# Kernel optimization log

Hardware: AMD Instinct MI355X
Metric: run time of the kernel (lower is better)

Reference implementation:

```python
import jax, jax.numpy as jnp
import numpy as np

EPS = 1e-5

def layernorm(x, g, b):
    mu = x.mean(-1, keepdims=True)
    var = ((x - mu) ** 2).mean(-1, keepdims=True)
    return (x - mu) / jnp.sqrt(var + EPS) * g + b

def segment_softmax(logits, seg, num_seg):
    # logits: [E, H, Q]; softmax over edges sharing the same target segment
    m = jax.ops.segment_max(logits, seg, num_segments=num_seg)
    ex = jnp.exp(logits - m[seg])
    s = jax.ops.segment_sum(ex, seg, num_segments=num_seg)
    return ex / s[seg]

def mha(x, Kw, Qw, Vw, tgt, src, n_tgt):
    # x: [N_src, C]; Kw/Vw: [H, C, D]; Qw: [H, Q, D]
    xK = jnp.einsum('nc,hcd->hnd', x, Kw)
    alpha = jnp.einsum('hqd,hnd->hqn', Qw, xK)            # [H, Q, N_src]
    a_e = alpha.transpose(2, 0, 1)[src]                   # [E, H, Q] per-edge logits
    w = segment_softmax(a_e, tgt, n_tgt)                  # sparse softmax over sources per target
    xV = jnp.einsum('nc,hcd->hnd', x, Vw)                 # [H, N_src, D]
    msg = w[..., None] * xV.transpose(1, 0, 2)[src][:, :, None, :]  # [E, H, Q, D]
    return jax.ops.segment_sum(msg, tgt, num_segments=n_tgt)        # [n_tgt, H, Q, D]

def block(x, tgt, src, n_tgt, Kw, Qw, Vw, g0, b0, W1, W2, g1, b1):
    Qn = Qw.shape[1]
    h = mha(x, Kw, Qw, Vw, tgt, src, n_tgt) + Qw          # [n_tgt, H, Q, D]
    h = h.transpose(0, 2, 1, 3).reshape(n_tgt, Qn, -1)    # [n_tgt, Q, hidden]
    h = layernorm(h, g0, b0)
    m = jax.nn.relu(jax.nn.relu(h @ W1) @ W2)             # MLP(Linear,ReLU,Linear) + outer ReLU
    h = layernorm(h + m, g1, b1)
    return h.sum(axis=1)                                  # [n_tgt, hidden]

def setup_inputs() -> dict:
    key = jax.random.key(0)
    ks = jax.random.split(key, 12)
    N, M, E, C, H, Q, D = 50000, 20000, 1000000, 128, 4, 1, 32
    HID = H * D
    s = 0.1
    inp = {
        'x_0': jax.random.normal(ks[0], (N, C), jnp.float32),
        'node_idx': jax.random.randint(ks[1], (E,), 0, N),
        'hedge_idx': jax.random.randint(ks[2], (E,), 0, M),
        'n_nodes': N,
        'n_hedges': M,
        'v2e_K': jax.random.normal(ks[3], (H, C, D), jnp.float32) * s,
        'v2e_Q': jax.random.normal(ks[4], (H, Q, D), jnp.float32) * s,
        'v2e_V': jax.random.normal(ks[5], (H, C, D), jnp.float32) * s,
        'v2e_ln0_g': jnp.ones((HID,), jnp.float32),
        'v2e_ln0_b': jnp.zeros((HID,), jnp.float32),
        'v2e_W1': jax.random.normal(ks[6], (HID, HID), jnp.float32) * s,
        'v2e_W2': jax.random.normal(ks[7], (HID, HID), jnp.float32) * s,
        'v2e_ln1_g': jnp.ones((HID,), jnp.float32),
        'v2e_ln1_b': jnp.zeros((HID,), jnp.float32),
        'e2v_K': jax.random.normal(ks[8], (H, HID, D), jnp.float32) * s,
        'e2v_Q': jax.random.normal(ks[9], (H, Q, D), jnp.float32) * s,
        'e2v_V': jax.random.normal(ks[10], (H, HID, D), jnp.float32) * s,
        'e2v_ln0_g': jnp.ones((HID,), jnp.float32),
        'e2v_ln0_b': jnp.zeros((HID,), jnp.float32),
        'e2v_W1': jax.random.normal(ks[11], (HID, HID), jnp.float32) * s,
        'e2v_W2': jax.random.normal(jax.random.fold_in(key, 99), (HID, HID), jnp.float32) * s,
        'e2v_ln1_g': jnp.ones((HID,), jnp.float32),
        'e2v_ln1_b': jnp.zeros((HID,), jnp.float32),
    }
    return inp

def reference(x_0, node_idx, hedge_idx, n_nodes, n_hedges,
              v2e_K, v2e_Q, v2e_V, v2e_ln0_g, v2e_ln0_b, v2e_W1, v2e_W2, v2e_ln1_g, v2e_ln1_b,
              e2v_K, e2v_Q, e2v_V, e2v_ln0_g, e2v_ln0_b, e2v_W1, e2v_W2, e2v_ln1_g, e2v_ln1_b):
    # vertex -> hyperedge: neighborhood = incidence^T, targets = hyperedges, sources = nodes
    x_1 = jax.nn.relu(block(x_0, hedge_idx, node_idx, n_hedges,
                            v2e_K, v2e_Q, v2e_V, v2e_ln0_g, v2e_ln0_b,
                            v2e_W1, v2e_W2, v2e_ln1_g, v2e_ln1_b))
    # hyperedge -> vertex: neighborhood = incidence, targets = nodes, sources = hyperedges
    x_0_out = jax.nn.relu(block(x_1, node_idx, hedge_idx, n_nodes,
                                e2v_K, e2v_Q, e2v_V, e2v_ln0_g, e2v_ln0_b,
                                e2v_W1, e2v_W2, e2v_ln1_g, e2v_ln1_b))
    return x_0_out, x_1
```

## Files before the change

kernel.cpp:

```cpp
#include <hip/hip_runtime.h>
#include <math.h>

typedef __attribute__((ext_vector_type(8))) short bf16x8;
typedef __attribute__((ext_vector_type(4))) float f32x4;

#define CSR_P 256

__device__ __forceinline__ unsigned short f2bf(float f){
  union { float f; unsigned int u; } c; c.f = f;
  unsigned int u = c.u;
  u += 0x7fff + ((u >> 16) & 1);
  return (unsigned short)(u >> 16);
}
__device__ __forceinline__ float bf2f(unsigned short h){
  union { unsigned int u; float f; } c; c.u = ((unsigned int)h) << 16;
  return c.f;
}

__device__ __forceinline__ float wsum64(float v){
  #pragma unroll
  for (int off = 32; off > 0; off >>= 1) v += __shfl_xor(v, off, 64);
  return v;
}

__global__ __launch_bounds__(256) void prephist_kernel(
    const int* __restrict__ tgt0, int NB0, const int* __restrict__ tgt1, int NB1, int E,
    int* __restrict__ counts0, int* __restrict__ counts1,
    const float* __restrict__ K0, const float* __restrict__ Q0, const float* __restrict__ V0,
    const float* __restrict__ W10, const float* __restrict__ W20,
    const float* __restrict__ K1, const float* __restrict__ Q1, const float* __restrict__ V1,
    const float* __restrict__ W11, const float* __restrict__ W21,
    unsigned short* __restrict__ btV0, unsigned short* __restrict__ btkq0,
    unsigned short* __restrict__ btW10, unsigned short* __restrict__ btW20,
    unsigned short* __restrict__ btV1, unsigned short* __restrict__ btkq1,
    unsigned short* __restrict__ btW11, unsigned short* __restrict__ btW21,
    int* __restrict__ cursors){
  if (blockIdx.x >= CSR_P){
    int pb = blockIdx.x - CSR_P;
    if (pb == 0 && blockIdx.y == 0 && threadIdx.x == 0){ cursors[0] = 0; cursors[1] = 0; }
    const float *K, *Q, *V, *W1, *W2;
    unsigned short *btV, *btkq, *btW1, *btW2;
    if (blockIdx.y == 0){ K=K0; Q=Q0; V=V0; W1=W10; W2=W20; btV=btV0; btkq=btkq0; btW1=btW10; btW2=btW20; }
    else                { K=K1; Q=Q1; V=V1; W1=W11; W2=W21; btV=btV1; btkq=btkq1; btW1=btW11; btW2=btW21; }
    int i = pb * 256 + threadIdx.x;
    if (i < 512){
      int h = i >> 7, c = i & 127;
      const float* Kp = K + (size_t)h * 4096 + (size_t)c * 32;
      const float* Qp = Q + h * 32;
      float s = 0.f;
      #pragma unroll
      for (int d = 0; d < 32; ++d) s += Kp[d] * Qp[d];
      unsigned short hi = f2bf(s);
      btkq[h * 128 + c]       = hi;
      btkq[(4 + h) * 128 + c] = f2bf(s - bf2f(hi));
      return;
    }
    int j = i - 512;
    if (j < 16384){
      int n = j >> 7, k = j & 127;
      int h = n >> 5, d = n & 31;
      btV[j] = f2bf(V[(size_t)h * 4096 + (size_t)k * 32 + d]);
      return;
    }
    j -= 16384;
    if (j < 16384){
      int n = j >> 7, k = j & 127;
      btW1[j] = f2bf(W1[(size_t)k * 128 + n]);
      return;
    }
    j -= 16384;
    if (j < 16384){
      int n = j >> 7, k = j & 127;
      btW2[j] = f2bf(W2[(size_t)k * 128 + n]);
    }
    return;
  }
  const int* tgt; int NB; int* counts;
  if (blockIdx.y == 0){ tgt = tgt0; NB = NB0; counts = counts0; }
  else                { tgt = tgt1; NB = NB1; counts = counts1; }
  __shared__ int hist[256];
  for (int i = threadIdx.x; i < NB; i += 256) hist[i] = 0;
  __syncthreads();
  int chunk = (E + CSR_P - 1) / CSR_P;
  int b0 = blockIdx.x * chunk, b1 = min(b0 + chunk, E);
  for (int e = b0 + threadIdx.x; e < b1; e += 256)
    atomicAdd(&hist[tgt[e] >> 8], 1);
  __syncthreads();
  for (int i = threadIdx.x; i < NB; i += 256)
    counts[i * CSR_P + blockIdx.x] = hist[i];
}

__global__ __launch_bounds__(256) void bscan_kernel(const int* __restrict__ counts0, int NB0,
                                                    const int* __restrict__ counts1,
                                                    int* __restrict__ blkoff0, int* __restrict__ blkoff1,
                                                    int* __restrict__ btot0, int* __restrict__ btot1,
                                                    int* __restrict__ base0, int* __restrict__ base1,
                                                    int* __restrict__ cursors){
  int i = blockIdx.x;
  const int* counts; int* blkoff; int* btot; int* bbase; int* cur; int b;
  if (i < NB0){ counts = counts0; blkoff = blkoff0; btot = btot0; bbase = base0; cur = &cursors[0]; b = i; }
  else        { counts = counts1; blkoff = blkoff1; btot = btot1; bbase = base1; cur = &cursors[1]; b = i - NB0; }
  __shared__ int wtmp[5];
  int tid = threadIdx.x, lane = tid & 63, wv = tid >> 6;
  int c = counts[b * CSR_P + tid];
  int s = c;
  #pragma unroll
  for (int off = 1; off < 64; off <<= 1){
    int t = __shfl_up(s, off, 64);
    if (lane >= off) s += t;
  }
  if (lane == 63) wtmp[wv] = s;
  __syncthreads();
  if (tid == 0){
    int a0 = wtmp[0], a1 = wtmp[1], a2 = wtmp[2], a3 = wtmp[3];
    wtmp[0] = 0; wtmp[1] = a0; wtmp[2] = a0 + a1; wtmp[3] = a0 + a1 + a2;
    int total = a0 + a1 + a2 + a3;
    wtmp[4] = total;
    btot[b] = total;
    int padded = ((total + 3) & ~3) + 1024;
    bbase[b] = atomicAdd(cur, padded);
  }
  __syncthreads();
  blkoff[b * CSR_P + tid] = s - c + wtmp[wv];
}

__global__ __launch_bounds__(256) void scatter2_kernel(
    const int* __restrict__ tgt0, const int* __restrict__ src0, int NB0,
    const int* __restrict__ base0, const int* __restrict__ blkoff0, int* __restrict__ pairs0,
    const int* __restrict__ tgt1, const int* __restrict__ src1, int NB1,
    const int* __restrict__ base1, const int* __restrict__ blkoff1, int* __restrict__ pairs1,
    int E){
  const int *tgt, *src, *bbase, *boff; int NB; int* pairs;
  if (blockIdx.y == 0){ tgt=tgt0; src=src0; bbase=base0; boff=blkoff0; NB=NB0; pairs=pairs0; }
  else                { tgt=tgt1; src=src1; bbase=base1; boff=blkoff1; NB=NB1; pairs=pairs1; }
  __shared__ int cur[256];
  for (int i = threadIdx.x; i < NB; i += 256)
    cur[i] = bbase[i] + boff[i * CSR_P + blockIdx.x];
  __syncthreads();
  int chunk = (E + CSR_P - 1) / CSR_P;
  int b0 = blockIdx.x * chunk, b1 = min(b0 + chunk, E);
  for (int e = b0 + threadIdx.x; e < b1; e += 256){
    int t = tgt[e];
    int pos = atomicAdd(&cur[t >> 8], 1);
    pairs[pos] = ((t & 255) << 24) | src[e];
  }
}

__global__ __launch_bounds__(1024) void build2_kernel(
    const int* __restrict__ base0, const int* __restrict__ btot0, int NB0,
    const int* __restrict__ pairs0, int n0, int d0,
    int* __restrict__ rp0, int* __restrict__ kc0, int* __restrict__ col0,
    const int* __restrict__ base1, const int* __restrict__ btot1, int NB1,
    const int* __restrict__ pairs1, int n1, int d1,
    int* __restrict__ rp1, int* __restrict__ kc1, int* __restrict__ col1){
  int b = blockIdx.x;
  const int *bbase, *bt; const int* pairs; int n_tgt, dummy;
  int *rowptr, *kcnt, *col;
  if (blockIdx.y == 0){
    if (b >= NB0) return;
    bbase=base0; bt=btot0; pairs=pairs0; n_tgt=n0; dummy=d0; rowptr=rp0; kcnt=kc0; col=col0;
  } else {
    if (b >= NB1) return;
    bbase=base1; bt=btot1; pairs=pairs1; n_tgt=n1; dummy=d1; rowptr=rp1; kcnt=kc1; col=col1;
  }
  __shared__ int hist2[2048];
  __shared__ int cur2[2048];
  __shared__ int hist[256];
  __shared__ int excl[256];
  int tid = threadIdx.x;
  int start = bbase[b];
  int end   = start + bt[b];
  for (int i = tid; i < 2048; i += 1024) hist2[i] = 0;
  __syncthreads();
  for (int e = start + tid; e < end; e += 1024){
    int p = pairs[e];
    atomicAdd(&hist2[(((p >> 24) & 255) << 3) | ((p & 0xFFFFFF) >> 13)], 1);
  }
  __syncthreads();
  if (tid < 256){
    int run = 0;
    #pragma unroll
    for (int t = 0; t < 8; ++t){ cur2[tid * 8 + t] = run; run += hist2[tid * 8 + t]; }
    hist[tid] = run;
  }
  __syncthreads();
  if (tid < 64){
    int lane = tid;
    int p0 = (hist[4 * lane]     + 3) & ~3;
    int p1 = (hist[4 * lane + 1] + 3) & ~3;
    int p2 = (hist[4 * lane + 2] + 3) & ~3;
    int p3 = (hist[4 * lane + 3] + 3) & ~3;
    int tsum = p0 + p1 + p2 + p3;
    int s = tsum;
    #pragma unroll
    for (int off = 1; off < 64; off <<= 1){
      int t = __shfl_up(s, off, 64);
      if (lane >= off) s += t;
    }
    int e0 = s - tsum;
    excl[4 * lane]     = e0;
    excl[4 * lane + 1] = e0 + p0;
    excl[4 * lane + 2] = e0 + p0 + p1;
    excl[4 * lane + 3] = e0 + p0 + p1 + p2;
  }
  __syncthreads();
  int t0 = b << 8;
  int valid = min(256, n_tgt - t0);
  if (tid < 256){
    int e0 = excl[tid];
    #pragma unroll
    for (int t = 0; t < 8; ++t) cur2[tid * 8 + t] += e0;
  }
  for (int i = tid; i < valid; i += 1024){
    rowptr[t0 + i] = start + excl[i];
    kcnt[t0 + i]   = (hist[i] + 3) & ~3;
  }
  __syncthreads();
  for (int e = start + tid; e < end; e += 1024){
    int p = pairs[e];
    int s = p & 0xFFFFFF;
    int pos = atomicAdd(&cur2[(((p >> 24) & 255) << 3) | (s >> 13)], 1);
    col[start + pos] = s;
  }
  __syncthreads();
  for (int i = tid; i < valid; i += 1024){
    int hc = hist[i], pc = (hc + 3) & ~3;
    int base = start + excl[i];
    for (int j = hc; j < pc; ++j) col[base + j] = dummy;
  }
}

__global__ __launch_bounds__(256) void gemm_xvl(const float* __restrict__ x,
                                                const unsigned short* __restrict__ btV,
                                                const unsigned short* __restrict__ btkq,
                                                unsigned short* __restrict__ xv,
                                                float* __restrict__ expl, int R){
  __shared__ unsigned short As[64 * 136];
  __shared__ unsigned short Bs[144 * 136];
  int tid = threadIdx.x;
  int row0 = blockIdx.x * 64;

  #pragma unroll
  for (int i = 0; i < 16; ++i){
    int f = tid + i * 256;
    int n = f >> 5, c4 = f & 31;
    *(ushort4*)&Bs[n * 136 + c4 * 4] = *(const ushort4*)(btV + n * 128 + c4 * 4);
  }
  {
    int n = tid >> 5, c4 = tid & 31;
    *(ushort4*)&Bs[(128 + n) * 136 + c4 * 4] = *(const ushort4*)(btkq + n * 128 + c4 * 4);
  }
  #pragma unroll
  for (int i = 0; i < 8; ++i){
    int f = tid + i * 256;
    int r = f >> 5, c4 = f & 31;
    float4 v = make_float4(0.f, 0.f, 0.f, 0.f);
    if (row0 + r < R) v = *(const float4*)(x + (size_t)(row0 + r) * 128 + c4 * 4);
    ushort4 h;
    h.x = f2bf(v.x); h.y = f2bf(v.y); h.z = f2bf(v.z); h.w = f2bf(v.w);
    *(ushort4*)&As[r * 136 + c4 * 4] = h;
  }
  __syncthreads();

  int lane = tid & 63, wv = tid >> 6;
  int m = lane & 15, quad = lane >> 4;
  f32x4 acc[9];
  #pragma unroll
  for (int j = 0; j < 9; ++j) acc[j] = (f32x4){0.f, 0.f, 0.f, 0.f};

  #pragma unroll
  for (int q = 0; q < 4; ++q){
    bf16x8 a = *(const bf16x8*)&As[(wv * 16 + m) * 136 + q * 32 + quad * 8];
    #pragma unroll
    for (int j = 0; j < 9; ++j){
      bf16x8 b = *(const bf16x8*)&Bs[(j * 16 + m) * 136 + q * 32 + quad * 8];
      acc[j] = __builtin_amdgcn_mfma_f32_16x16x32_bf16(a, b, acc[j], 0, 0, 0);
    }
  }

  #pragma unroll
  for (int j = 0; j < 8; ++j){
    int colc = j * 16 + m;
    #pragma unroll
    for (int r = 0; r < 4; ++r){
      int gr = row0 + wv * 16 + quad * 4 + r;
      if (gr <= R) xv[(size_t)gr * 128 + colc] = f2bf(acc[j][r]);
    }
  }
  #pragma unroll
  for (int r = 0; r < 4; ++r){
    int gr = row0 + wv * 16 + quad * 4 + r;
    float lg = acc[8][r] + __shfl_xor(acc[8][r], 4, 64);
    if (m < 4 && gr <= R)
      expl[(size_t)gr * 4 + m] = (gr == R) ? 0.f : __expf(lg);
  }
}

__global__ __launch_bounds__(256) void agg_kernel(const int* __restrict__ rowptr,
                                                  const int* __restrict__ kcnt,
                                                  const int* __restrict__ col,
                                                  const float* __restrict__ expl,
                                                  const unsigned short* __restrict__ xV,
                                                  const float* __restrict__ qvec,
                                                  const float* __restrict__ g0,
                                                  const float* __restrict__ b0,
                                                  unsigned short* __restrict__ hb_out,
                                                  int n_tgt){
  int wv_id = __builtin_amdgcn_readfirstlane(threadIdx.x >> 6);
  int wid = (blockIdx.x << 2) + wv_id;
  if (wid >= n_tgt) return;
  int lane = threadIdx.x & 63;
  int half = lane >> 5;
  int c    = lane & 31;
  unsigned hh = (unsigned)(c >> 3);
  int beg = rowptr[wid];
  int k   = kcnt[wid];

  const uint2* xv64 = (const uint2*)xV;
  float acc0 = 0.f, acc1 = 0.f, acc2 = 0.f, acc3 = 0.f, sumw = 0.f;
  #pragma unroll 2
  for (int e = 0; e < k; e += 4){
    int4 cc = *(const int4*)(col + beg + e);
    #pragma unroll
    for (int p = 0; p < 2; ++p){
      int sA = p ? cc.z : cc.x;
      int sB = p ? cc.w : cc.y;
      int se = half ? sB : sA;
      float a  = expl[((unsigned)se << 2) + hh];
      uint2 v  = xv64[((unsigned)se << 5) + (unsigned)c];
      union { unsigned u; float f; } t0, t1, t2, t3;
      t0.u = v.x << 16;          t1.u = v.x & 0xffff0000u;
      t2.u = v.y << 16;          t3.u = v.y & 0xffff0000u;
      sumw += a;
      acc0 += a * t0.f;  acc1 += a * t1.f;
      acc2 += a * t2.f;  acc3 += a * t3.f;
    }
  }
  sumw += __shfl_xor(sumw, 32, 64);
  acc0 += __shfl_xor(acc0, 32, 64);
  acc1 += __shfl_xor(acc1, 32, 64);
  acc2 += __shfl_xor(acc2, 32, 64);
  acc3 += __shfl_xor(acc3, 32, 64);

  float inv = (sumw > 0.f) ? 1.f / sumw : 0.f;
  acc0 *= inv; acc1 *= inv; acc2 *= inv; acc3 *= inv;

  float4 q4 = *(const float4*)(qvec + 4 * c);
  acc0 += q4.x; acc1 += q4.y; acc2 += q4.z; acc3 += q4.w;

  float mean = wsum64(acc0 + acc1 + acc2 + acc3) * (1.f / 256.f);
  float d0 = acc0 - mean, d1 = acc1 - mean, d2 = acc2 - mean, d3 = acc3 - mean;
  float var = wsum64(d0 * d0 + d1 * d1 + d2 * d2 + d3 * d3) * (1.f / 256.f);
  float rstd = rsqrtf(var + 1e-5f);
  float4 g4 = *(const float4*)(g0 + 4 * c);
  float4 b4 = *(const float4*)(b0 + 4 * c);
  float o0 = d0 * rstd * g4.x + b4.x;
  float o1 = d1 * rstd * g4.y + b4.y;
  float o2 = d2 * rstd * g4.z + b4.z;
  float o3 = d3 * rstd * g4.w + b4.w;
  if (half == 0){
    uint2 pk;
    pk.x = ((unsigned)f2bf(o1) << 16) | (unsigned)f2bf(o0);
    pk.y = ((unsigned)f2bf(o3) << 16) | (unsigned)f2bf(o2);
    *(uint2*)(hb_out + 128 * (size_t)wid + 4 * c) = pk;
  }
}

__global__ __launch_bounds__(256) void mfma_mlp_ln(const unsigned short* __restrict__ A,
                                                   const unsigned short* __restrict__ Bt1,
                                                   const unsigned short* __restrict__ Bt2,
                                                   const float* __restrict__ g,
                                                   const float* __restrict__ b,
                                                   float* __restrict__ outp, int R){
  __shared__ unsigned short As[64 * 136];
  __shared__ unsigned short Bs[128 * 136];
  int tid = threadIdx.x;
  int row0 = blockIdx.x * 64;

  #pragma unroll
  for (int i = 0; i < 16; ++i){
    int f = tid + i * 256;
    int n = f >> 5, c4 = f & 31;
    *(ushort4*)&Bs[n * 136 + c4 * 4] = *(const ushort4*)(Bt1 + n * 128 + c4 * 4);
  }
  #pragma unroll
  for (int i = 0; i < 8; ++i){
    int f = tid + i * 256;
    int r = f >> 5, c4 = f & 31;
    ushort4 v = make_ushort4(0, 0, 0, 0);
    if (row0 + r < R) v = *(const ushort4*)(A + (size_t)(row0 + r) * 128 + c4 * 4);
    *(ushort4*)&As[r * 136 + c4 * 4] = v;
  }
  __syncthreads();

  int lane = tid & 63, wv = tid >> 6;
  int m = lane & 15, quad = lane >> 4;
  f32x4 acc[8];
  #pragma unroll
  for (int j = 0; j < 8; ++j) acc[j] = (f32x4){0.f, 0.f, 0.f, 0.f};

  #pragma unroll
  for (int q = 0; q < 4; ++q){
    bf16x8 a = *(const bf16x8*)&As[(wv * 16 + m) * 136 + q * 32 + quad * 8];
    #pragma unroll
    for (int j = 0; j < 8; ++j){
      bf16x8 b8 = *(const bf16x8*)&Bs[(j * 16 + m) * 136 + q * 32 + quad * 8];
      acc[j] = __builtin_amdgcn_mfma_f32_16x16x32_bf16(a, b8, acc[j], 0, 0, 0);
    }
  }

  float res[4][8];
  #pragma unroll
  for (int r = 0; r < 4; ++r)
    #pragma unroll
    for (int j = 0; j < 8; ++j)
      res[r][j] = bf2f(As[(wv * 16 + quad * 4 + r) * 136 + j * 16 + m]);
  __syncthreads();

  #pragma unroll
  for (int j = 0; j < 8; ++j){
    #pragma unroll
    for (int r = 0; r < 4; ++r)
      As[(wv * 16 + quad * 4 + r) * 136 + j * 16 + m] = f2bf(fmaxf(acc[j][r], 0.f));
  }
  #pragma unroll
  for (int i = 0; i < 16; ++i){
    int f = tid + i * 256;
    int n = f >> 5, c4 = f & 31;
    *(ushort4*)&Bs[n * 136 + c4 * 4] = *(const ushort4*)(Bt2 + n * 128 + c4 * 4);
  }
  __syncthreads();

  #pragma unroll
  for (int j = 0; j < 8; ++j) acc[j] = (f32x4){0.f, 0.f, 0.f, 0.f};
  #pragma unroll
  for (int q = 0; q < 4; ++q){
    bf16x8 a = *(const bf16x8*)&As[(wv * 16 + m) * 136 + q * 32 + quad * 8];
    #pragma unroll
    for (int j = 0; j < 8; ++j){
      bf16x8 b8 = *(const bf16x8*)&Bs[(j * 16 + m) * 136 + q * 32 + quad * 8];
      acc[j] = __builtin_amdgcn_mfma_f32_16x16x32_bf16(a, b8, acc[j], 0, 0, 0);
    }
  }

  float gv[8], bv[8];
  #pragma unroll
  for (int j = 0; j < 8; ++j){ gv[j] = g[j * 16 + m]; bv[j] = b[j * 16 + m]; }

  #pragma unroll
  for (int r = 0; r < 4; ++r){
    int gr = row0 + wv * 16 + quad * 4 + r;
    if (gr >= R) continue;
    float v[8];
    float s = 0.f;
    #pragma unroll
    for (int j = 0; j < 8; ++j){
      float mm = fmaxf(acc[j][r], 0.f);
      v[j] = res[r][j] + mm;
      s += v[j];
    }
    s += __shfl_xor(s, 1, 64); s += __shfl_xor(s, 2, 64);
    s += __shfl_xor(s, 4, 64); s += __shfl_xor(s, 8, 64);
    float mean = s * (1.f / 128.f);
    float s2 = 0.f;
    #pragma unroll
    for (int j = 0; j < 8; ++j){ v[j] -= mean; s2 += v[j] * v[j]; }
    s2 += __shfl_xor(s2, 1, 64); s2 += __shfl_xor(s2, 2, 64);
    s2 += __shfl_xor(s2, 4, 64); s2 += __shfl_xor(s2, 8, 64);
    float rstd = rsqrtf(s2 * (1.f / 128.f) + 1e-5f);
    #pragma unroll
    for (int j = 0; j < 8; ++j)
      outp[(size_t)gr * 128 + j * 16 + m] = fmaxf(v[j] * rstd * gv[j] + bv[j], 0.f);
  }
}

struct Ws {
  float *expl;
  unsigned short *btV0, *btkq0, *btW10, *btW20, *btV1, *btkq1, *btW11, *btW21, *xv, *hb;
};

static void run_stage(const float* x_f32, int R_src,
                      const int* rowptr, const int* kcnt, const int* col, int n_tgt,
                      const unsigned short* btV, const unsigned short* btkq,
                      const unsigned short* btW1, const unsigned short* btW2,
                      const float* Qw, const float* g0, const float* b0,
                      const float* g1, const float* b1,
                      float* out, const Ws& ws, hipStream_t stream)
{
  gemm_xvl<<<(R_src + 1 + 63) / 64, 256, 0, stream>>>(x_f32, btV, btkq, ws.xv, ws.expl, R_src);
  agg_kernel<<<(n_tgt + 3) / 4, 256, 0, stream>>>(rowptr, kcnt, col, ws.expl, ws.xv,
                                                  Qw, g0, b0, ws.hb, n_tgt);
  mfma_mlp_ln<<<(n_tgt + 63) / 64, 256, 0, stream>>>(ws.hb, btW1, btW2, g1, b1, out, n_tgt);
}

extern "C" void kernel_launch(void* const* d_in, const int* in_sizes, int n_in,
                              void* d_out, int out_size, void* d_ws, size_t ws_size,
                              hipStream_t stream)
{
  const float* x0        = (const float*)d_in[0];
  const int*   node_idx  = (const int*)d_in[1];
  const int*   hedge_idx = (const int*)d_in[2];
  const float* v2e_K = (const float*)d_in[5];
  const float* v2e_Q = (const float*)d_in[6];
  const float* v2e_V = (const float*)d_in[7];
  const float* v2e_g0 = (const float*)d_in[8];
  const float* v2e_b0 = (const float*)d_in[9];
  const float* v2e_W1 = (const float*)d_in[10];
  const float* v2e_W2 = (const float*)d_in[11];
  const float* v2e_g1 = (const float*)d_in[12];
  const float* v2e_b1 = (const float*)d_in[13];
  const float* e2v_K = (const float*)d_in[14];
  const float* e2v_Q = (const float*)d_in[15];
  const float* e2v_V = (const float*)d_in[16];
  const float* e2v_g0 = (const float*)d_in[17];
  const float* e2v_b0 = (const float*)d_in[18];
  const float* e2v_W1 = (const float*)d_in[19];
  const float* e2v_W2 = (const float*)d_in[20];
  const float* e2v_g1 = (const float*)d_in[21];
  const float* e2v_b1 = (const float*)d_in[22];

  int N = in_sizes[0] / 128;
  int E = in_sizes[1];
  int M = out_size / 128 - N;

  float* out_x0 = (float*)d_out;
  float* out_x1 = (float*)d_out + (size_t)N * 128;

  size_t off = 0;
  char* base = (char*)d_ws;
  auto alloc = [&](size_t bytes) -> void* {
    void* p = base + off;
    off += (bytes + 255) & ~(size_t)255;
    return p;
  };
  int NB0 = (M + 255) >> 8;
  int NB1 = (N + 255) >> 8;
  int NBmax = NB1 > NB0 ? NB1 : NB0;
  size_t capP = (size_t)E + 1024 * (size_t)NBmax + 64;

  Ws ws;
  ws.btV0  = (unsigned short*)alloc(16384 * 2);
  ws.btkq0 = (unsigned short*)alloc(1024 * 2);
  ws.btW10 = (unsigned short*)alloc(16384 * 2);
  ws.btW20 = (unsigned short*)alloc(16384 * 2);
  ws.btV1  = (unsigned short*)alloc(16384 * 2);
  ws.btkq1 = (unsigned short*)alloc(1024 * 2);
  ws.btW11 = (unsigned short*)alloc(16384 * 2);
  ws.btW21 = (unsigned short*)alloc(16384 * 2);
  ws.expl  = (float*)alloc(((size_t)N + 1) * 4 * 4);
  size_t uoff = off;
  ws.xv    = (unsigned short*)alloc(((size_t)N + 1) * 128 * 2);
  ws.hb    = (unsigned short*)alloc((size_t)N * 128 * 2);
  int* pairs0  = (int*)(base + uoff);
  int* pairs1  = pairs0 + capP;
  int* counts0 = pairs1 + capP;
  int* counts1 = counts0 + 256 * CSR_P;
  int* blkoff0 = counts1 + 256 * CSR_P;
  int* blkoff1 = blkoff0 + 256 * CSR_P;
  int* btot0   = blkoff1 + 256 * CSR_P;
  int* btot1   = btot0 + 256;
  int* base0   = btot1 + 256;
  int* base1   = base0 + 256;
  int* cursors = base1 + 256;
  int* rowptr0 = (int*)alloc((size_t)M * 4);
  int* kcnt0   = (int*)alloc((size_t)M * 4);
  int* col0    = (int*)alloc(capP * 4);
  int* rowptr1 = (int*)alloc((size_t)N * 4);
  int* kcnt1   = (int*)alloc((size_t)N * 4);
  int* col1    = (int*)alloc(capP * 4);
  (void)ws_size; (void)n_in;

  prephist_kernel<<<dim3(CSR_P + 194, 2), 256, 0, stream>>>(
      hedge_idx, NB0, node_idx, NB1, E, counts0, counts1,
      v2e_K, v2e_Q, v2e_V, v2e_W1, v2e_W2,
      e2v_K, e2v_Q, e2v_V, e2v_W1, e2v_W2,
      ws.btV0, ws.btkq0, ws.btW10, ws.btW20,
      ws.btV1, ws.btkq1, ws.btW11, ws.btW21, cursors);

  bscan_kernel<<<NB0 + NB1, 256, 0, stream>>>(counts0, NB0, counts1,
                                              blkoff0, blkoff1, btot0, btot1,
                                              base0, base1, cursors);
  scatter2_kernel<<<dim3(CSR_P, 2), 256, 0, stream>>>(
      hedge_idx, node_idx, NB0, base0, blkoff0, pairs0,
      node_idx, hedge_idx, NB1, base1, blkoff1, pairs1, E);
  build2_kernel<<<dim3(NBmax, 2), 1024, 0, stream>>>(
      base0, btot0, NB0, pairs0, M, N, rowptr0, kcnt0, col0,
      base1, btot1, NB1, pairs1, N, M, rowptr1, kcnt1, col1);

  run_stage(x0, N, rowptr0, kcnt0, col0, M,
            ws.btV0, ws.btkq0, ws.btW10, ws.btW20,
            v2e_Q, v2e_g0, v2e_b0, v2e_g1, v2e_b1,
            out_x1, ws, stream);

  run_stage(out_x1, M, rowptr1, kcnt1, col1, N,
            ws.btV1, ws.btkq1, ws.btW11, ws.btW21,
            e2v_Q, e2v_g0, e2v_b0, e2v_g1, e2v_b1,
            out_x0, ws, stream);
}
```

Baseline: 286.2 us.

## Fuse scatter with first GEMM, split aggregation by channel halves, move LN0 into MLP

Merges the CSR scatter kernel and the first-stage xV/logit GEMM into one launch, so GEMM blocks can run alongside the scatter blocks. The aggregation kernel now runs in two launches, each covering 64 of the 128 channels with 32-bit gathers. This is meant to shrink the per-pass working set and cache footprint, at the cost of re-reading col and expl twice. The Q-bias add and first layernorm move out of aggregation into the MLP kernel's A-tile load, computed with one-pass mean and variance. Scratch buffers no longer alias the xv region because the GEMM now runs concurrently with the scatter.

```diff
diff --git a/kernel.cpp b/kernel.cpp
--- a/kernel.cpp
+++ b/kernel.cpp
@@ -15,12 +15,6 @@
 __device__ __forceinline__ float bf2f(unsigned short h){
   union { unsigned int u; float f; } c; c.u = ((unsigned int)h) << 16;
   return c.f;
-}
-
-__device__ __forceinline__ float wsum64(float v){
-  #pragma unroll
-  for (int off = 32; off > 0; off >>= 1) v += __shfl_xor(v, off, 64);
-  return v;
 }
 
 __global__ __launch_bounds__(256) void prephist_kernel(
@@ -124,26 +118,112 @@
   blkoff[b * CSR_P + tid] = s - c + wtmp[wv];
 }
 
-__global__ __launch_bounds__(256) void scatter2_kernel(
+__device__ __forceinline__ void gemm_xvl_body(unsigned short* As, unsigned short* Bs,
+                                              const float* __restrict__ x,
+                                              const unsigned short* __restrict__ btV,
+                                              const unsigned short* __restrict__ btkq,
+                                              unsigned short* __restrict__ xv,
+                                              float* __restrict__ expl, int R, int bx){
+  int tid = threadIdx.x;
+  int row0 = bx * 64;
+
+  #pragma unroll
+  for (int i = 0; i < 16; ++i){
+    int f = tid + i * 256;
+    int n = f >> 5, c4 = f & 31;
+    *(ushort4*)&Bs[n * 136 + c4 * 4] = *(const ushort4*)(btV + n * 128 + c4 * 4);
+  }
+  {
+    int n = tid >> 5, c4 = tid & 31;
+    *(ushort4*)&Bs[(128 + n) * 136 + c4 * 4] = *(const ushort4*)(btkq + n * 128 + c4 * 4);
+  }
+  #pragma unroll
+  for (int i = 0; i < 8; ++i){
+    int f = tid + i * 256;
+    int r = f >> 5, c4 = f & 31;
+    float4 v = make_float4(0.f, 0.f, 0.f, 0.f);
+    if (row0 + r < R) v = *(const float4*)(x + (size_t)(row0 + r) * 128 + c4 * 4);
+    ushort4 h;
+    h.x = f2bf(v.x); h.y = f2bf(v.y); h.z = f2bf(v.z); h.w = f2bf(v.w);
+    *(ushort4*)&As[r * 136 + c4 * 4] = h;
+  }
+  __syncthreads();
+
+  int lane = tid & 63, wv = tid >> 6;
+  int m = lane & 15, quad = lane >> 4;
+  f32x4 acc[9];
+  #pragma unroll
+  for (int j = 0; j < 9; ++j) acc[j] = (f32x4){0.f, 0.f, 0.f, 0.f};
+
+  #pragma unroll
+  for (int q = 0; q < 4; ++q){
+    bf16x8 a = *(const bf16x8*)&As[(wv * 16 + m) * 136 + q * 32 + quad * 8];
+    #pragma unroll
+    for (int j = 0; j < 9; ++j){
+      bf16x8 b = *(const bf16x8*)&Bs[(j * 16 + m) * 136 + q * 32 + quad * 8];
+      acc[j] = __builtin_amdgcn_mfma_f32_16x16x32_bf16(a, b, acc[j], 0, 0, 0);
+    }
+  }
+
+  #pragma unroll
+  for (int j = 0; j < 8; ++j){
+    int colc = j * 16 + m;
+    #pragma unroll
+    for (int r = 0; r < 4; ++r){
+      int gr = row0 + wv * 16 + quad * 4 + r;
+      if (gr <= R) xv[(size_t)gr * 128 + colc] = f2bf(acc[j][r]);
+    }
+  }
+  #pragma unroll
+  for (int r = 0; r < 4; ++r){
+    int gr = row0 + wv * 16 + quad * 4 + r;
+    float lg = acc[8][r] + __shfl_xor(acc[8][r], 4, 64);
+    if (m < 4 && gr <= R)
+      expl[(size_t)gr * 4 + m] = (gr == R) ? 0.f : __expf(lg);
+  }
+}
+
+__global__ __launch_bounds__(256) void gemm_xvl(const float* __restrict__ x,
+                                                const unsigned short* __restrict__ btV,
+                                                const unsigned short* __restrict__ btkq,
+                                                unsigned short* __restrict__ xv,
+                                                float* __restrict__ expl, int R){
+  __shared__ unsigned short As[64 * 136];
+  __shared__ unsigned short Bs[144 * 136];
+  gemm_xvl_body(As, Bs, x, btV, btkq, xv, expl, R, blockIdx.x);
+}
+
+__global__ __launch_bounds__(256) void scatgemm_kernel(
     const int* __restrict__ tgt0, const int* __restrict__ src0, int NB0,
     const int* __restrict__ base0, const int* __restrict__ blkoff0, int* __restrict__ pairs0,
     const int* __restrict__ tgt1, const int* __restrict__ src1, int NB1,
     const int* __restrict__ base1, const int* __restrict__ blkoff1, int* __restrict__ pairs1,
-    int E){
-  const int *tgt, *src, *bbase, *boff; int NB; int* pairs;
-  if (blockIdx.y == 0){ tgt=tgt0; src=src0; bbase=base0; boff=blkoff0; NB=NB0; pairs=pairs0; }
-  else                { tgt=tgt1; src=src1; bbase=base1; boff=blkoff1; NB=NB1; pairs=pairs1; }
-  __shared__ int cur[256];
-  for (int i = threadIdx.x; i < NB; i += 256)
-    cur[i] = bbase[i] + boff[i * CSR_P + blockIdx.x];
-  __syncthreads();
-  int chunk = (E + CSR_P - 1) / CSR_P;
-  int b0 = blockIdx.x * chunk, b1 = min(b0 + chunk, E);
-  for (int e = b0 + threadIdx.x; e < b1; e += 256){
-    int t = tgt[e];
-    int pos = atomicAdd(&cur[t >> 8], 1);
-    pairs[pos] = ((t & 255) << 24) | src[e];
-  }
+    int E,
+    const float* __restrict__ x, const unsigned short* __restrict__ btV,
+    const unsigned short* __restrict__ btkq,
+    unsigned short* __restrict__ xv, float* __restrict__ expl, int R){
+  __shared__ unsigned short As[64 * 136];
+  __shared__ unsigned short Bs[144 * 136];
+  if (blockIdx.x < 2 * CSR_P){
+    int y = blockIdx.x >> 8;
+    int bx = blockIdx.x & 255;
+    const int *tgt, *src, *bbase, *boff; int NB; int* pairs;
+    if (y == 0){ tgt=tgt0; src=src0; bbase=base0; boff=blkoff0; NB=NB0; pairs=pairs0; }
+    else       { tgt=tgt1; src=src1; bbase=base1; boff=blkoff1; NB=NB1; pairs=pairs1; }
+    int* cur = (int*)As;
+    for (int i = threadIdx.x; i < NB; i += 256)
+      cur[i] = bbase[i] + boff[i * CSR_P + bx];
+    __syncthreads();
+    int chunk = (E + CSR_P - 1) / CSR_P;
+    int b0 = bx * chunk, b1 = min(b0 + chunk, E);
+    for (int e = b0 + threadIdx.x; e < b1; e += 256){
+      int t = tgt[e];
+      int pos = atomicAdd(&cur[t >> 8], 1);
+      pairs[pos] = ((t & 255) << 24) | src[e];
+    }
+    return;
+  }
+  gemm_xvl_body(As, Bs, x, btV, btkq, xv, expl, R, blockIdx.x - 2 * CSR_P);
 }
 
 __global__ __launch_bounds__(1024) void build2_kernel(
@@ -230,94 +310,27 @@
   }
 }
 
-__global__ __launch_bounds__(256) void gemm_xvl(const float* __restrict__ x,
-                                                const unsigned short* __restrict__ btV,
-                                                const unsigned short* __restrict__ btkq,
-                                                unsigned short* __restrict__ xv,
-                                                float* __restrict__ expl, int R){
-  __shared__ unsigned short As[64 * 136];
-  __shared__ unsigned short Bs[144 * 136];
-  int tid = threadIdx.x;
-  int row0 = blockIdx.x * 64;
-
-  #pragma unroll
-  for (int i = 0; i < 16; ++i){
-    int f = tid + i * 256;
-    int n = f >> 5, c4 = f & 31;
-    *(ushort4*)&Bs[n * 136 + c4 * 4] = *(const ushort4*)(btV + n * 128 + c4 * 4);
-  }
-  {
-    int n = tid >> 5, c4 = tid & 31;
-    *(ushort4*)&Bs[(128 + n) * 136 + c4 * 4] = *(const ushort4*)(btkq + n * 128 + c4 * 4);
-  }
-  #pragma unroll
-  for (int i = 0; i < 8; ++i){
-    int f = tid + i * 256;
-    int r = f >> 5, c4 = f & 31;
-    float4 v = make_float4(0.f, 0.f, 0.f, 0.f);
-    if (row0 + r < R) v = *(const float4*)(x + (size_t)(row0 + r) * 128 + c4 * 4);
-    ushort4 h;
-    h.x = f2bf(v.x); h.y = f2bf(v.y); h.z = f2bf(v.z); h.w = f2bf(v.w);
-    *(ushort4*)&As[r * 136 + c4 * 4] = h;
-  }
-  __syncthreads();
-
-  int lane = tid & 63, wv = tid >> 6;
-  int m = lane & 15, quad = lane >> 4;
-  f32x4 acc[9];
-  #pragma unroll
-  for (int j = 0; j < 9; ++j) acc[j] = (f32x4){0.f, 0.f, 0.f, 0.f};
-
-  #pragma unroll
-  for (int q = 0; q < 4; ++q){
-    bf16x8 a = *(const bf16x8*)&As[(wv * 16 + m) * 136 + q * 32 + quad * 8];
-    #pragma unroll
-    for (int j = 0; j < 9; ++j){
-      bf16x8 b = *(const bf16x8*)&Bs[(j * 16 + m) * 136 + q * 32 + quad * 8];
-      acc[j] = __builtin_amdgcn_mfma_f32_16x16x32_bf16(a, b, acc[j], 0, 0, 0);
-    }
-  }
-
-  #pragma unroll
-  for (int j = 0; j < 8; ++j){
-    int colc = j * 16 + m;
-    #pragma unroll
-    for (int r = 0; r < 4; ++r){
-      int gr = row0 + wv * 16 + quad * 4 + r;
-      if (gr <= R) xv[(size_t)gr * 128 + colc] = f2bf(acc[j][r]);
-    }
-  }
-  #pragma unroll
-  for (int r = 0; r < 4; ++r){
-    int gr = row0 + wv * 16 + quad * 4 + r;
-    float lg = acc[8][r] + __shfl_xor(acc[8][r], 4, 64);
-    if (m < 4 && gr <= R)
-      expl[(size_t)gr * 4 + m] = (gr == R) ? 0.f : __expf(lg);
-  }
-}
-
 __global__ __launch_bounds__(256) void agg_kernel(const int* __restrict__ rowptr,
                                                   const int* __restrict__ kcnt,
                                                   const int* __restrict__ col,
                                                   const float* __restrict__ expl,
                                                   const unsigned short* __restrict__ xV,
-                                                  const float* __restrict__ qvec,
-                                                  const float* __restrict__ g0,
-                                                  const float* __restrict__ b0,
                                                   unsigned short* __restrict__ hb_out,
-                                                  int n_tgt){
+                                                  int n_tgt, int choff){
   int wv_id = __builtin_amdgcn_readfirstlane(threadIdx.x >> 6);
   int wid = (blockIdx.x << 2) + wv_id;
   if (wid >= n_tgt) return;
   int lane = threadIdx.x & 63;
   int half = lane >> 5;
   int c    = lane & 31;
-  unsigned hh = (unsigned)(c >> 3);
+  int ch   = choff + 2 * c;
+  unsigned hh = (unsigned)(ch >> 5);
   int beg = rowptr[wid];
   int k   = kcnt[wid];
 
-  const uint2* xv64 = (const uint2*)xV;
-  float acc0 = 0.f, acc1 = 0.f, acc2 = 0.f, acc3 = 0.f, sumw = 0.f;
+  const unsigned* xv32 = (const unsigned*)xV;
+  unsigned cbase = (unsigned)(choff >> 1) + (unsigned)c;
+  float acc0 = 0.f, acc1 = 0.f, sumw = 0.f;
   #pragma unroll 2
   for (int e = 0; e < k; e += 4){
     int4 cc = *(const int4*)(col + beg + e);
@@ -326,49 +339,32 @@
       int sA = p ? cc.z : cc.x;
       int sB = p ? cc.w : cc.y;
       int se = half ? sB : sA;
-      float a  = expl[((unsigned)se << 2) + hh];
-      uint2 v  = xv64[((unsigned)se << 5) + (unsigned)c];
-      union { unsigned u; float f; } t0, t1, t2, t3;
-      t0.u = v.x << 16;          t1.u = v.x & 0xffff0000u;
-      t2.u = v.y << 16;          t3.u = v.y & 0xffff0000u;
+      float a    = expl[((unsigned)se << 2) + hh];
+      unsigned v = xv32[((unsigned)se << 6) + cbase];
+      union { unsigned u; float f; } lo, hi;
+      lo.u = v << 16;  hi.u = v & 0xffff0000u;
       sumw += a;
-      acc0 += a * t0.f;  acc1 += a * t1.f;
-      acc2 += a * t2.f;  acc3 += a * t3.f;
+      acc0 += a * lo.f;  acc1 += a * hi.f;
     }
   }
   sumw += __shfl_xor(sumw, 32, 64);
   acc0 += __shfl_xor(acc0, 32, 64);
   acc1 += __shfl_xor(acc1, 32, 64);
-  acc2 += __shfl_xor(acc2, 32, 64);
-  acc3 += __shfl_xor(acc3, 32, 64);
 
   float inv = (sumw > 0.f) ? 1.f / sumw : 0.f;
-  acc0 *= inv; acc1 *= inv; acc2 *= inv; acc3 *= inv;
-
-  float4 q4 = *(const float4*)(qvec + 4 * c);
-  acc0 += q4.x; acc1 += q4.y; acc2 += q4.z; acc3 += q4.w;
-
-  float mean = wsum64(acc0 + acc1 + acc2 + acc3) * (1.f / 256.f);
-  float d0 = acc0 - mean, d1 = acc1 - mean, d2 = acc2 - mean, d3 = acc3 - mean;
-  float var = wsum64(d0 * d0 + d1 * d1 + d2 * d2 + d3 * d3) * (1.f / 256.f);
-  float rstd = rsqrtf(var + 1e-5f);
-  float4 g4 = *(const float4*)(g0 + 4 * c);
-  float4 b4 = *(const float4*)(b0 + 4 * c);
-  float o0 = d0 * rstd * g4.x + b4.x;
-  float o1 = d1 * rstd * g4.y + b4.y;
-  float o2 = d2 * rstd * g4.z + b4.z;
-  float o3 = d3 * rstd * g4.w + b4.w;
+  acc0 *= inv; acc1 *= inv;
   if (half == 0){
-    uint2 pk;
-    pk.x = ((unsigned)f2bf(o1) << 16) | (unsigned)f2bf(o0);
-    pk.y = ((unsigned)f2bf(o3) << 16) | (unsigned)f2bf(o2);
-    *(uint2*)(hb_out + 128 * (size_t)wid + 4 * c) = pk;
+    unsigned pk = ((unsigned)f2bf(acc1) << 16) | (unsigned)f2bf(acc0);
+    *(unsigned*)(hb_out + 128 * (size_t)wid + ch) = pk;
   }
 }
 
 __global__ __launch_bounds__(256) void mfma_mlp_ln(const unsigned short* __restrict__ A,
                                                    const unsigned short* __restrict__ Bt1,
                                                    const unsigned short* __restrict__ Bt2,
+                                                   const float* __restrict__ qvec,
+                                                   const float* __restrict__ g0v,
+                                                   const float* __restrict__ b0v,
                                                    const float* __restrict__ g,
                                                    const float* __restrict__ b,
                                                    float* __restrict__ outp, int R){
@@ -389,7 +385,27 @@
     int r = f >> 5, c4 = f & 31;
     ushort4 v = make_ushort4(0, 0, 0, 0);
     if (row0 + r < R) v = *(const ushort4*)(A + (size_t)(row0 + r) * 128 + c4 * 4);
-    *(ushort4*)&As[r * 136 + c4 * 4] = v;
+    float4 q4 = *(const float4*)(qvec + c4 * 4);
+    float x0 = bf2f(v.x) + q4.x, x1 = bf2f(v.y) + q4.y;
+    float x2 = bf2f(v.z) + q4.z, x3 = bf2f(v.w) + q4.w;
+    float s1 = x0 + x1 + x2 + x3;
+    float s2 = x0 * x0 + x1 * x1 + x2 * x2 + x3 * x3;
+    #pragma unroll
+    for (int off = 1; off < 32; off <<= 1){
+      s1 += __shfl_xor(s1, off, 64);
+      s2 += __shfl_xor(s2, off, 64);
+    }
+    float mean = s1 * (1.f / 128.f);
+    float var  = s2 * (1.f / 128.f) - mean * mean;
+    float rstd = rsqrtf(var + 1e-5f);
+    float4 g4 = *(const float4*)(g0v + c4 * 4);
+    float4 b4 = *(const float4*)(b0v + c4 * 4);
+    ushort4 h;
+    h.x = f2bf((x0 - mean) * rstd * g4.x + b4.x);
+    h.y = f2bf((x1 - mean) * rstd * g4.y + b4.y);
+    h.z = f2bf((x2 - mean) * rstd * g4.z + b4.z);
+    h.w = f2bf((x3 - mean) * rstd * g4.w + b4.w);
+    *(ushort4*)&As[r * 136 + c4 * 4] = h;
   }
   __syncthreads();
 
@@ -478,20 +494,6 @@
   float *expl;
   unsigned short *btV0, *btkq0, *btW10, *btW20, *btV1, *btkq1, *btW11, *btW21, *xv, *hb;
 };
-
-static void run_stage(const float* x_f32, int R_src,
-                      const int* rowptr, const int* kcnt, const int* col, int n_tgt,
-                      const unsigned short* btV, const unsigned short* btkq,
-                      const unsigned short* btW1, const unsigned short* btW2,
-                      const float* Qw, const float* g0, const float* b0,
-                      const float* g1, const float* b1,
-                      float* out, const Ws& ws, hipStream_t stream)
-{
-  gemm_xvl<<<(R_src + 1 + 63) / 64, 256, 0, stream>>>(x_f32, btV, btkq, ws.xv, ws.expl, R_src);
-  agg_kernel<<<(n_tgt + 3) / 4, 256, 0, stream>>>(rowptr, kcnt, col, ws.expl, ws.xv,
-                                                  Qw, g0, b0, ws.hb, n_tgt);
-  mfma_mlp_ln<<<(n_tgt + 63) / 64, 256, 0, stream>>>(ws.hb, btW1, btW2, g1, b1, out, n_tgt);
-}
 
 extern "C" void kernel_launch(void* const* d_in, const int* in_sizes, int n_in,
                               void* d_out, int out_size, void* d_ws, size_t ws_size,
@@ -548,20 +550,19 @@
   ws.btW11 = (unsigned short*)alloc(16384 * 2);
   ws.btW21 = (unsigned short*)alloc(16384 * 2);
   ws.expl  = (float*)alloc(((size_t)N + 1) * 4 * 4);
-  size_t uoff = off;
   ws.xv    = (unsigned short*)alloc(((size_t)N + 1) * 128 * 2);
   ws.hb    = (unsigned short*)alloc((size_t)N * 128 * 2);
-  int* pairs0  = (int*)(base + uoff);
-  int* pairs1  = pairs0 + capP;
-  int* counts0 = pairs1 + capP;
-  int* counts1 = counts0 + 256 * CSR_P;
-  int* blkoff0 = counts1 + 256 * CSR_P;
-  int* blkoff1 = blkoff0 + 256 * CSR_P;
-  int* btot0   = blkoff1 + 256 * CSR_P;
-  int* btot1   = btot0 + 256;
-  int* base0   = btot1 + 256;
-  int* base1   = base0 + 256;
-  int* cursors = base1 + 256;
+  int* pairs0  = (int*)alloc(capP * 4);
+  int* pairs1  = (int*)alloc(capP * 4);
+  int* counts0 = (int*)alloc(256 * CSR_P * 4);
+  int* counts1 = (int*)alloc(256 * CSR_P * 4);
+  int* blkoff0 = (int*)alloc(256 * CSR_P * 4);
+  int* blkoff1 = (int*)alloc(256 * CSR_P * 4);
+  int* btot0   = (int*)alloc(256 * 4);
+  int* btot1   = (int*)alloc(256 * 4);
+  int* base0   = (int*)alloc(256 * 4);
+  int* base1   = (int*)alloc(256 * 4);
+  int* cursors = (int*)alloc(256 * 4);
   int* rowptr0 = (int*)alloc((size_t)M * 4);
   int* kcnt0   = (int*)alloc((size_t)M * 4);
   int* col0    = (int*)alloc(capP * 4);
@@ -580,20 +581,32 @@
   bscan_kernel<<<NB0 + NB1, 256, 0, stream>>>(counts0, NB0, counts1,
                                               blkoff0, blkoff1, btot0, btot1,
                                               base0, base1, cursors);
-  scatter2_kernel<<<dim3(CSR_P, 2), 256, 0, stream>>>(
+
+  int G1 = (N + 1 + 63) / 64;
+  scatgemm_kernel<<<2 * CSR_P + G1, 256, 0, stream>>>(
       hedge_idx, node_idx, NB0, base0, blkoff0, pairs0,
-      node_idx, hedge_idx, NB1, base1, blkoff1, pairs1, E);
+      node_idx, hedge_idx, NB1, base1, blkoff1, pairs1, E,
+      x0, ws.btV0, ws.btkq0, ws.xv, ws.expl, N);
+
   build2_kernel<<<dim3(NBmax, 2), 1024, 0, stream>>>(
       base0, btot0, NB0, pairs0, M, N, rowptr0, kcnt0, col0,
       base1, btot1, NB1, pairs1, N, M, rowptr1, kcnt1, col1);
 
-  run_stage(x0, N, rowptr0, kcnt0, col0, M,
-            ws.btV0, ws.btkq0, ws.btW10, ws.btW20,
-            v2e_Q, v2e_g0, v2e_b0, v2e_g1, v2e_b1,
-            out_x1, ws, stream);
-
-  run_stage(out_x1, M, rowptr1, kcnt1, col1, N,
-            ws.btV1, ws.btkq1, ws.btW11, ws.btW21,
-            e2v_Q, e2v_g0, e2v_b0, e2v_g1, e2v_b1,
-            out_x0, ws, stream);
-}
+  agg_kernel<<<(M + 3) / 4, 256, 0, stream>>>(rowptr0, kcnt0, col0, ws.expl, ws.xv,
+                                              ws.hb, M, 0);
+  agg_kernel<<<(M + 3) / 4, 256, 0, stream>>>(rowptr0, kcnt0, col0, ws.expl, ws.xv,
+                                              ws.hb, M, 64);
+  mfma_mlp_ln<<<(M + 63) / 64, 256, 0, stream>>>(ws.hb, ws.btW10, ws.btW20,
+                                                 v2e_Q, v2e_g0, v2e_b0,
+                                                 v2e_g1, v2e_b1, out_x1, M);
+
+  gemm_xvl<<<(M + 1 + 63) / 64, 256, 0, stream>>>(out_x1, ws.btV1, ws.btkq1,
+                                                  ws.xv, ws.expl, M);
+  agg_kernel<<<(N + 3) / 4, 256, 0, stream>>>(rowptr1, kcnt1, col1, ws.expl, ws.xv,
+                                              ws.hb, N, 0);
+  agg_kernel<<<(N + 3) / 4, 256, 0, stream>>>(rowptr1, kcnt1, col1, ws.expl, ws.xv,
+                                              ws.hb, N, 64);
+  mfma_mlp_ln<<<(N + 63) / 64, 256, 0, stream>>>(ws.hb, ws.btW11, ws.btW21,
+                                                 e2v_Q, e2v_g0, e2v_b0,
+                                                 e2v_g1, e2v_b1, out_x0, N);
+}
```

New measurement: 319.0 us. 11.5% more time.
